# Kernel tuning notes

Hardware: AMD Instinct MI355X
Metric: run time of the kernel (lower is better)

## Reference

```python
import jax, jax.numpy as jnp
import numpy as np

B, L, D, H, A = 4, 2048, 1024, 16, 64  # batch, seq, d_model, n_head, d_head


def setup_inputs() -> dict:
    key = jax.random.key(0)
    ks = jax.random.split(key, 6)
    scale = 1.0 / np.sqrt(D)
    return {
        "xq": jax.random.normal(ks[0], (B, L, D), dtype=jnp.float32),
        "xkv": jax.random.normal(ks[1], (B, L, D), dtype=jnp.float32),
        "Q": jax.random.normal(ks[2], (D, H, A), dtype=jnp.float32) * scale,
        "K": jax.random.normal(ks[3], (D, H, A), dtype=jnp.float32) * scale,
        "V": jax.random.normal(ks[4], (D, H, A), dtype=jnp.float32) * scale,
        "O": jax.random.normal(ks[5], (D, H, A), dtype=jnp.float32) * scale,
    }


def reference(xq, xkv, Q, K, V, O):
    # embed: 'dha, ...ld -> ...lha'
    q = jnp.einsum('dha,bld->blha', Q, xq)
    k = jnp.einsum('dha,bld->blha', K, xkv)
    v = jnp.einsum('dha,bld->blha', V, xkv)
    # outer: '...lha, ...mha -> ...hlm'  (full LxL score matrix, no scaling in source)
    scores = jnp.einsum('blha,bmha->bhlm', q, k)
    attn = jax.nn.softmax(scores, axis=-1)  # dropout p=0 (eval)
    # score: '...hlm, ...mha -> ...lha'
    ctx = jnp.einsum('bhlm,bmha->blha', attn, v)
    # output: '...dha, ...lha -> ...ld'
    return jnp.einsum('dha,blha->bld', O, ctx)
```

## Files before the change

### kernel.cpp

```cpp
#include <hip/hip_runtime.h>
#include <math.h>

typedef __bf16 bf16;
typedef bf16 bf16x8 __attribute__((ext_vector_type(8)));
typedef bf16 bf16x4 __attribute__((ext_vector_type(4)));
typedef float f32x4 __attribute__((ext_vector_type(4)));
typedef float f32x16 __attribute__((ext_vector_type(16)));

#define B_ 4
#define L_ 2048
#define D_ 1024
#define H_ 16
#define A_ 64
#define HA_ 1024
#define BL_ 8192
#define LOG2E 1.44269504088896340736f

__device__ __forceinline__ void gload16(const void* g, void* l) {
  __builtin_amdgcn_global_load_lds((const __attribute__((address_space(1))) void*)g,
                                   (__attribute__((address_space(3))) void*)l,
                                   16, 0, 0);
}

__device__ __forceinline__ unsigned cvt_pk_bf16(float lo, float hi) {
  unsigned r;
  asm volatile("v_cvt_pk_bf16_f32 %0, %1, %2" : "=v"(r) : "v"(lo), "v"(hi));
  return r;
}

__device__ __forceinline__ void permswap(unsigned& a, unsigned& b) {
  asm volatile("v_permlane32_swap_b32 %0, %1" : "+v"(a), "+v"(b));
}

__device__ __forceinline__ void half_pair(float x, float& o1, float& o2) {
  unsigned a = __builtin_bit_cast(unsigned, x), b;
  asm volatile("v_mov_b32 %0, %1" : "=v"(b) : "v"(a));
  asm volatile("v_permlane32_swap_b32 %0, %1" : "+v"(a), "+v"(b));
  o1 = __builtin_bit_cast(float, a);
  o2 = __builtin_bit_cast(float, b);
}

__global__ __launch_bounds__(256) void cast_all(const float* __restrict__ xq,
                                                const float* __restrict__ xkv,
                                                const float* __restrict__ ow,
                                                bf16* __restrict__ xq_b,
                                                bf16* __restrict__ xkv_b,
                                                bf16* __restrict__ wo_b) {
  const int NX = BL_ * D_ / 8;
  const int NW = D_ * HA_ / 8;
  int i = blockIdx.x * blockDim.x + threadIdx.x;
  const float* src;
  bf16* dst;
  int j;
  if (i < NX) { src = xq; dst = xq_b; j = i; }
  else if (i < 2 * NX) { src = xkv; dst = xkv_b; j = i - NX; }
  else if (i < 2 * NX + NW) { src = ow; dst = wo_b; j = i - 2 * NX; }
  else return;
  const float4* s = reinterpret_cast<const float4*>(src) + (size_t)j * 2;
  float4 a = s[0], b = s[1];
  bf16x8 o;
  o[0] = (bf16)a.x; o[1] = (bf16)a.y; o[2] = (bf16)a.z; o[3] = (bf16)a.w;
  o[4] = (bf16)b.x; o[5] = (bf16)b.y; o[6] = (bf16)b.z; o[7] = (bf16)b.w;
  *reinterpret_cast<bf16x8*>(dst + (size_t)j * 8) = o;
}

__global__ __launch_bounds__(256) void transpose_cast_w3(const float* __restrict__ wq,
                                                         const float* __restrict__ wk,
                                                         const float* __restrict__ wv,
                                                         bf16* __restrict__ oq,
                                                         bf16* __restrict__ ok,
                                                         bf16* __restrict__ ov) {
  __shared__ float tile[32][33];
  const int z = blockIdx.z;
  const float* w = (z == 0) ? wq : (z == 1) ? wk : wv;
  bf16* wt = (z == 0) ? oq : (z == 1) ? ok : ov;
  const float scale = (z == 0) ? LOG2E : 1.0f;
  const int d0 = blockIdx.y * 32, h0 = blockIdx.x * 32;
  const int tx = threadIdx.x, ty = threadIdx.y;
  #pragma unroll
  for (int j = 0; j < 4; j++)
    tile[ty + j * 8][tx] = w[(size_t)(d0 + ty + j * 8) * HA_ + h0 + tx];
  __syncthreads();
  #pragma unroll
  for (int j = 0; j < 4; j++)
    wt[(size_t)(h0 + ty + j * 8) * D_ + d0 + tx] = (bf16)(tile[tx][ty + j * 8] * scale);
}

template <int MODE>
__device__ __forceinline__ void gemm_bt_core(const bf16* __restrict__ Ap,
                                             const bf16* __restrict__ Bp,
                                             void* __restrict__ Cp,
                                             int m0, int n0) {
  const int K = 1024;
  __shared__ __align__(16) bf16 As[128 * 32];
  __shared__ __align__(16) bf16 Bs[128 * 32];
  const int tid = threadIdx.x;
  const int lane = tid & 63, w = tid >> 6;
  const int wr = w >> 1, wc = w & 1;
  const int g = lane >> 4, c = lane & 15;
  f32x4 acc[4][4] = {};
  const int srow = tid >> 2, sch = tid & 3;
  const int sw0 = (sch ^ (srow & 3)) * 8;
  for (int k0 = 0; k0 < K; k0 += 32) {
    gload16(Ap + (size_t)(m0 + srow) * K + k0 + sw0, As + tid * 8);
    gload16(Ap + (size_t)(m0 + 64 + srow) * K + k0 + sw0, As + (256 + tid) * 8);
    gload16(Bp + (size_t)(n0 + srow) * K + k0 + sw0, Bs + tid * 8);
    gload16(Bp + (size_t)(n0 + 64 + srow) * K + k0 + sw0, Bs + (256 + tid) * 8);
    __syncthreads();
    bf16x8 af[4], bfr[4];
    #pragma unroll
    for (int m = 0; m < 4; m++)
      af[m] = *reinterpret_cast<const bf16x8*>(As + (wr * 64 + m * 16 + c) * 32 + ((g ^ (c & 3)) * 8));
    #pragma unroll
    for (int n = 0; n < 4; n++)
      bfr[n] = *reinterpret_cast<const bf16x8*>(Bs + (wc * 64 + n * 16 + c) * 32 + ((g ^ (c & 3)) * 8));
    #pragma unroll
    for (int m = 0; m < 4; m++)
      #pragma unroll
      for (int n = 0; n < 4; n++)
        acc[m][n] = __builtin_amdgcn_mfma_f32_16x16x32_bf16(af[m], bfr[n], acc[m][n], 0, 0, 0);
    __syncthreads();
  }
  #pragma unroll
  for (int m = 0; m < 4; m++) {
    #pragma unroll
    for (int n = 0; n < 4; n++) {
      if (MODE == 2) {
        int row0 = m0 + wr * 64 + m * 16 + g * 4;
        int col = n0 + wc * 64 + n * 16 + c;
        int b = row0 >> 11, l0 = row0 & 2047, h = col >> 6, a = col & 63;
        bf16x4 o4;
        #pragma unroll
        for (int i = 0; i < 4; i++) o4[i] = (bf16)acc[m][n][i];
        *reinterpret_cast<bf16x4*>((bf16*)Cp + ((size_t)(b * H_ + h) * A_ + a) * L_ + l0) = o4;
      } else {
        #pragma unroll
        for (int i = 0; i < 4; i++) {
          int row = m0 + wr * 64 + m * 16 + g * 4 + i;
          int col = n0 + wc * 64 + n * 16 + c;
          float v = acc[m][n][i];
          if (MODE == 0) {
            int b = row >> 11, l = row & 2047, h = col >> 6, a = col & 63;
            ((bf16*)Cp)[(((size_t)b * H_ + h) * L_ + l) * A_ + a] = (bf16)v;
          } else {
            ((float*)Cp)[(size_t)row * 1024 + col] = v;
          }
        }
      }
    }
  }
}

__device__ __forceinline__ void xcd_mn(int id, int& m0, int& n0) {
  int xcd = id & 7, j = id >> 3;
  m0 = (xcd * 8 + (j >> 3)) * 128;
  n0 = (j & 7) * 128;
}

__global__ __launch_bounds__(256, 2) void gemm_proj(const bf16* xq_b, const bf16* xkv_b,
                                                    const bf16* wq, const bf16* wk, const bf16* wv,
                                                    bf16* qb, bf16* kb, bf16* vtb) {
  int m0, n0;
  xcd_mn(blockIdx.x, m0, n0);
  const int z = blockIdx.z;
  if (z == 0)      gemm_bt_core<0>(xq_b, wq, qb, m0, n0);
  else if (z == 1) gemm_bt_core<0>(xkv_b, wk, kb, m0, n0);
  else             gemm_bt_core<2>(xkv_b, wv, vtb, m0, n0);
}

__global__ __launch_bounds__(256, 2) void gemm_out_k(const bf16* ctx, const bf16* wo, float* out) {
  int m0, n0;
  xcd_mn(blockIdx.x, m0, n0);
  gemm_bt_core<1>(ctx, wo, out, m0, n0);
}

__device__ __forceinline__ void pa_build(const f32x16& s, bf16x8& f0, bf16x8& f1) {
  #pragma unroll
  for (int sl = 0; sl < 2; sl++) {
    unsigned a0 = cvt_pk_bf16(s[8 * sl + 0], s[8 * sl + 1]);
    unsigned b0 = cvt_pk_bf16(s[8 * sl + 4], s[8 * sl + 5]);
    permswap(a0, b0);
    unsigned a1 = cvt_pk_bf16(s[8 * sl + 2], s[8 * sl + 3]);
    unsigned b1 = cvt_pk_bf16(s[8 * sl + 6], s[8 * sl + 7]);
    permswap(a1, b1);
    uint4 v; v.x = a0; v.y = a1; v.z = b0; v.w = b1;
    if (sl == 0) f0 = __builtin_bit_cast(bf16x8, v);
    else         f1 = __builtin_bit_cast(bf16x8, v);
  }
}

__global__ __launch_bounds__(512, 2) void attn_kernel(const bf16* __restrict__ qg,
                                                      const bf16* __restrict__ kg,
                                                      const bf16* __restrict__ vtg,
                                                      bf16* __restrict__ ctx) {
  __shared__ __align__(16) bf16 Ks[2][64 * 64];
  __shared__ __align__(16) bf16 Vs[2][64 * 64];
  const int tid = threadIdx.x;
  const int lane = tid & 63;
  const int w = tid >> 6;
  const int c = lane & 31;
  const int hi = lane >> 5;
  const int cs7 = c & 7;
  const int bh = blockIdx.x;
  const int q0 = blockIdx.y * 256;
  const bf16* qh = qg + (size_t)bh * L_ * A_;
  const bf16* kh = kg + (size_t)bh * L_ * A_;
  const bf16* vh = vtg + (size_t)bh * A_ * L_;

  const int qrow = q0 + w * 32 + c;
  bf16x8 qf[4];
  #pragma unroll
  for (int ds = 0; ds < 4; ds++)
    qf[ds] = *reinterpret_cast<const bf16x8*>(qh + (size_t)qrow * A_ + ds * 16 + hi * 8);

  f32x16 oacc0 = {}, oacc1 = {};
  float lrun = 0.f;

  int koA[4], koB[4];
  #pragma unroll
  for (int ds = 0; ds < 4; ds++) {
    koA[ds] = c * 64 + ((2 * ds + hi) ^ cs7) * 8;
    koB[ds] = (32 + c) * 64 + ((2 * ds + hi) ^ cs7) * 8;
  }

  const int sr = tid >> 3, sc = tid & 7;
  const int ss = (sc ^ (sr & 7)) * 8;
  const bf16* ksrc = kh + (size_t)sr * A_ + ss;
  const bf16* vsrc = vh + (size_t)sr * L_ + ss;

  gload16(ksrc, &Ks[0][tid * 8]);
  gload16(vsrc, &Vs[0][tid * 8]);
  __syncthreads();
  int cur = 0;

  for (int t = 0; t < L_ / 64; t++) {
    if (t < L_ / 64 - 1) {
      gload16(ksrc + (size_t)(t + 1) * 4096, &Ks[cur ^ 1][tid * 8]);
      gload16(vsrc + (size_t)(t + 1) * 64, &Vs[cur ^ 1][tid * 8]);
    }
    const bf16* Kc = Ks[cur];
    const bf16* Vc = Vs[cur];

    f32x16 s0 = {}, s1 = {};
    __builtin_amdgcn_s_setprio(1);
    #pragma unroll
    for (int ds = 0; ds < 4; ds++) {
      bf16x8 k0 = *reinterpret_cast<const bf16x8*>(Kc + koA[ds]);
      bf16x8 k1 = *reinterpret_cast<const bf16x8*>(Kc + koB[ds]);
      s0 = __builtin_amdgcn_mfma_f32_32x32x16_bf16(k0, qf[ds], s0, 0, 0, 0);
      s1 = __builtin_amdgcn_mfma_f32_32x32x16_bf16(k1, qf[ds], s1, 0, 0, 0);
    }
    __builtin_amdgcn_s_setprio(0);

    #pragma unroll
    for (int r = 0; r < 16; r++) {
      s0[r] = __builtin_amdgcn_exp2f(s0[r]);
      s1[r] = __builtin_amdgcn_exp2f(s1[r]);
    }

    float u0[8];
    #pragma unroll
    for (int r = 0; r < 8; r++)
      u0[r] = (s0[r] + s0[r + 8]) + (s1[r] + s1[r + 8]);
    float us = ((u0[0] + u0[1]) + (u0[2] + u0[3])) + ((u0[4] + u0[5]) + (u0[6] + u0[7]));
    float y1, y2;
    half_pair(us, y1, y2);
    lrun += y1 + y2;

    bf16x8 paf0, paf1, paf2, paf3;
    pa_build(s0, paf0, paf1);
    pa_build(s1, paf2, paf3);

    __builtin_amdgcn_s_setprio(1);
    #pragma unroll
    for (int ks = 0; ks < 4; ks++) {
      const bf16x8 pa = (ks == 0) ? paf0 : (ks == 1) ? paf1 : (ks == 2) ? paf2 : paf3;
      bf16x8 v0 = *reinterpret_cast<const bf16x8*>(Vc + koA[ks]);
      bf16x8 v1 = *reinterpret_cast<const bf16x8*>(Vc + koB[ks]);
      oacc0 = __builtin_amdgcn_mfma_f32_32x32x16_bf16(v0, pa, oacc0, 0, 0, 0);
      oacc1 = __builtin_amdgcn_mfma_f32_32x32x16_bf16(v1, pa, oacc1, 0, 0, 0);
    }
    __builtin_amdgcn_s_setprio(0);

    __syncthreads();
    cur ^= 1;
  }

  float inv = 1.f / lrun;
  const int b = bh >> 4, h = bh & 15;
  bf16* crow = ctx + (((size_t)b * L_ + qrow) * H_ + h) * A_;
  #pragma unroll
  for (int n = 0; n < 2; n++) {
    #pragma unroll
    for (int rq = 0; rq < 4; rq++) {
      bf16x4 o4;
      #pragma unroll
      for (int j = 0; j < 4; j++) {
        float v = (n == 0) ? oacc0[rq * 4 + j] : oacc1[rq * 4 + j];
        o4[j] = (bf16)(v * inv);
      }
      *reinterpret_cast<bf16x4*>(crow + n * 32 + rq * 8 + hi * 4) = o4;
    }
  }
}

extern "C" void kernel_launch(void* const* d_in, const int* in_sizes, int n_in,
                              void* d_out, int out_size, void* d_ws, size_t ws_size,
                              hipStream_t stream) {
  const float* xq = (const float*)d_in[0];
  const float* xkv = (const float*)d_in[1];
  const float* Qw = (const float*)d_in[2];
  const float* Kw = (const float*)d_in[3];
  const float* Vw = (const float*)d_in[4];
  const float* Ow = (const float*)d_in[5];
  float* out = (float*)d_out;

  char* ws = (char*)d_ws;
  const size_t SZ16 = (size_t)BL_ * HA_ * sizeof(bf16);
  const size_t SZW = (size_t)D_ * HA_ * sizeof(bf16);
  bf16* xq_b = (bf16*)(ws);
  bf16* xkv_b = (bf16*)(ws + SZ16);
  bf16* wq_t = (bf16*)(ws + 2 * SZ16);
  bf16* wk_t = (bf16*)(ws + 2 * SZ16 + SZW);
  bf16* wv_t = (bf16*)(ws + 2 * SZ16 + 2 * SZW);
  bf16* wo_b = (bf16*)(ws + 2 * SZ16 + 3 * SZW);
  bf16* qb = (bf16*)(ws + 2 * SZ16 + 4 * SZW);
  bf16* kb = qb + (size_t)BL_ * HA_;
  bf16* vtb = kb + (size_t)BL_ * HA_;
  bf16* ctxb = xkv_b;

  const int NCAST = (2 * BL_ * D_ + D_ * HA_) / 8;
  cast_all<<<(NCAST + 255) / 256, 256, 0, stream>>>(xq, xkv, Ow, xq_b, xkv_b, wo_b);
  transpose_cast_w3<<<dim3(32, 32, 3), dim3(32, 8), 0, stream>>>(Qw, Kw, Vw, wq_t, wk_t, wv_t);

  gemm_proj<<<dim3(512, 1, 3), 256, 0, stream>>>(xq_b, xkv_b, wq_t, wk_t, wv_t, qb, kb, vtb);
  attn_kernel<<<dim3(64, 8), 512, 0, stream>>>(qb, kb, vtb, ctxb);
  gemm_out_k<<<512, 256, 0, stream>>>(ctxb, wo_b, out);
}
```

Measured before the change: 192.3 us.

## Process two 32-row query tiles per wave in attention, halving block threads

The attention kernel now uses 256 threads per block, and each wave handles 64 query rows as two 32-row halves instead of 32 rows. Each K/V fragment read from LDS is reused for twice as many MFMAs, and each thread stages two 16-byte chunks of K and of V per tile. This cuts LDS read traffic and the number of waves per block synchronizing per tile. In exchange, register pressure per thread roughly doubles (accumulators and score tiles), which may hurt occupancy or cause spills.

```diff
diff --git a/kernel.cpp b/kernel.cpp
--- a/kernel.cpp
+++ b/kernel.cpp
@@ -189,7 +189,7 @@
   }
 }
 
-__global__ __launch_bounds__(512, 2) void attn_kernel(const bf16* __restrict__ qg,
+__global__ __launch_bounds__(256, 2) void attn_kernel(const bf16* __restrict__ qg,
                                                       const bf16* __restrict__ kg,
                                                       const bf16* __restrict__ vtg,
                                                       bf16* __restrict__ ctx) {
@@ -207,14 +207,18 @@
   const bf16* kh = kg + (size_t)bh * L_ * A_;
   const bf16* vh = vtg + (size_t)bh * A_ * L_;
 
-  const int qrow = q0 + w * 32 + c;
-  bf16x8 qf[4];
-  #pragma unroll
-  for (int ds = 0; ds < 4; ds++)
-    qf[ds] = *reinterpret_cast<const bf16x8*>(qh + (size_t)qrow * A_ + ds * 16 + hi * 8);
-
-  f32x16 oacc0 = {}, oacc1 = {};
-  float lrun = 0.f;
+  const int qrowL = q0 + w * 64 + c;
+  const int qrowH = qrowL + 32;
+  bf16x8 qfL[4], qfH[4];
+  #pragma unroll
+  for (int ds = 0; ds < 4; ds++) {
+    qfL[ds] = *reinterpret_cast<const bf16x8*>(qh + (size_t)qrowL * A_ + ds * 16 + hi * 8);
+    qfH[ds] = *reinterpret_cast<const bf16x8*>(qh + (size_t)qrowH * A_ + ds * 16 + hi * 8);
+  }
+
+  f32x16 oA0 = {}, oA1 = {};
+  f32x16 oB0 = {}, oB1 = {};
+  float lrunL = 0.f, lrunH = 0.f;
 
   int koA[4], koB[4];
   #pragma unroll
@@ -225,60 +229,81 @@
 
   const int sr = tid >> 3, sc = tid & 7;
   const int ss = (sc ^ (sr & 7)) * 8;
-  const bf16* ksrc = kh + (size_t)sr * A_ + ss;
-  const bf16* vsrc = vh + (size_t)sr * L_ + ss;
-
-  gload16(ksrc, &Ks[0][tid * 8]);
-  gload16(vsrc, &Vs[0][tid * 8]);
+  const bf16* ksrc0 = kh + (size_t)sr * A_ + ss;
+  const bf16* ksrc1 = kh + (size_t)(sr + 32) * A_ + ss;
+  const bf16* vsrc0 = vh + (size_t)sr * L_ + ss;
+  const bf16* vsrc1 = vh + (size_t)(sr + 32) * L_ + ss;
+
+  auto stage = [&](int buf, int t) {
+    gload16(ksrc0 + (size_t)t * 4096, &Ks[buf][tid * 8]);
+    gload16(ksrc1 + (size_t)t * 4096, &Ks[buf][2048 + tid * 8]);
+    gload16(vsrc0 + (size_t)t * 64, &Vs[buf][tid * 8]);
+    gload16(vsrc1 + (size_t)t * 64, &Vs[buf][2048 + tid * 8]);
+  };
+
+  stage(0, 0);
   __syncthreads();
   int cur = 0;
 
   for (int t = 0; t < L_ / 64; t++) {
-    if (t < L_ / 64 - 1) {
-      gload16(ksrc + (size_t)(t + 1) * 4096, &Ks[cur ^ 1][tid * 8]);
-      gload16(vsrc + (size_t)(t + 1) * 64, &Vs[cur ^ 1][tid * 8]);
-    }
+    if (t < L_ / 64 - 1) stage(cur ^ 1, t + 1);
     const bf16* Kc = Ks[cur];
     const bf16* Vc = Vs[cur];
 
-    f32x16 s0 = {}, s1 = {};
+    f32x16 sA0 = {}, sA1 = {}, sB0 = {}, sB1 = {};
     __builtin_amdgcn_s_setprio(1);
     #pragma unroll
     for (int ds = 0; ds < 4; ds++) {
       bf16x8 k0 = *reinterpret_cast<const bf16x8*>(Kc + koA[ds]);
       bf16x8 k1 = *reinterpret_cast<const bf16x8*>(Kc + koB[ds]);
-      s0 = __builtin_amdgcn_mfma_f32_32x32x16_bf16(k0, qf[ds], s0, 0, 0, 0);
-      s1 = __builtin_amdgcn_mfma_f32_32x32x16_bf16(k1, qf[ds], s1, 0, 0, 0);
+      sA0 = __builtin_amdgcn_mfma_f32_32x32x16_bf16(k0, qfL[ds], sA0, 0, 0, 0);
+      sA1 = __builtin_amdgcn_mfma_f32_32x32x16_bf16(k1, qfL[ds], sA1, 0, 0, 0);
+      sB0 = __builtin_amdgcn_mfma_f32_32x32x16_bf16(k0, qfH[ds], sB0, 0, 0, 0);
+      sB1 = __builtin_amdgcn_mfma_f32_32x32x16_bf16(k1, qfH[ds], sB1, 0, 0, 0);
     }
     __builtin_amdgcn_s_setprio(0);
 
     #pragma unroll
     for (int r = 0; r < 16; r++) {
-      s0[r] = __builtin_amdgcn_exp2f(s0[r]);
-      s1[r] = __builtin_amdgcn_exp2f(s1[r]);
-    }
-
-    float u0[8];
-    #pragma unroll
-    for (int r = 0; r < 8; r++)
-      u0[r] = (s0[r] + s0[r + 8]) + (s1[r] + s1[r + 8]);
-    float us = ((u0[0] + u0[1]) + (u0[2] + u0[3])) + ((u0[4] + u0[5]) + (u0[6] + u0[7]));
-    float y1, y2;
-    half_pair(us, y1, y2);
-    lrun += y1 + y2;
-
-    bf16x8 paf0, paf1, paf2, paf3;
-    pa_build(s0, paf0, paf1);
-    pa_build(s1, paf2, paf3);
+      sA0[r] = __builtin_amdgcn_exp2f(sA0[r]);
+      sA1[r] = __builtin_amdgcn_exp2f(sA1[r]);
+      sB0[r] = __builtin_amdgcn_exp2f(sB0[r]);
+      sB1[r] = __builtin_amdgcn_exp2f(sB1[r]);
+    }
+
+    {
+      float u0[8], v0[8];
+      #pragma unroll
+      for (int r = 0; r < 8; r++) {
+        u0[r] = (sA0[r] + sA0[r + 8]) + (sA1[r] + sA1[r + 8]);
+        v0[r] = (sB0[r] + sB0[r + 8]) + (sB1[r] + sB1[r + 8]);
+      }
+      float us = ((u0[0] + u0[1]) + (u0[2] + u0[3])) + ((u0[4] + u0[5]) + (u0[6] + u0[7]));
+      float vs = ((v0[0] + v0[1]) + (v0[2] + v0[3])) + ((v0[4] + v0[5]) + (v0[6] + v0[7]));
+      float y1, y2, z1, z2;
+      half_pair(us, y1, y2);
+      half_pair(vs, z1, z2);
+      lrunL += y1 + y2;
+      lrunH += z1 + z2;
+    }
+
+    bf16x8 paA0, paA1, paA2, paA3, paB0, paB1, paB2, paB3;
+    pa_build(sA0, paA0, paA1);
+    pa_build(sA1, paA2, paA3);
+    pa_build(sB0, paB0, paB1);
+    pa_build(sB1, paB2, paB3);
 
     __builtin_amdgcn_s_setprio(1);
     #pragma unroll
     for (int ks = 0; ks < 4; ks++) {
-      const bf16x8 pa = (ks == 0) ? paf0 : (ks == 1) ? paf1 : (ks == 2) ? paf2 : paf3;
+      const bf16x8 pa = (ks == 0) ? paA0 : (ks == 1) ? paA1 : (ks == 2) ? paA2 : paA3;
+      const bf16x8 pb = (ks == 0) ? paB0 : (ks == 1) ? paB1 : (ks == 2) ? paB2 : paB3;
       bf16x8 v0 = *reinterpret_cast<const bf16x8*>(Vc + koA[ks]);
       bf16x8 v1 = *reinterpret_cast<const bf16x8*>(Vc + koB[ks]);
-      oacc0 = __builtin_amdgcn_mfma_f32_32x32x16_bf16(v0, pa, oacc0, 0, 0, 0);
-      oacc1 = __builtin_amdgcn_mfma_f32_32x32x16_bf16(v1, pa, oacc1, 0, 0, 0);
+      oA0 = __builtin_amdgcn_mfma_f32_32x32x16_bf16(v0, pa, oA0, 0, 0, 0);
+      oA1 = __builtin_amdgcn_mfma_f32_32x32x16_bf16(v1, pa, oA1, 0, 0, 0);
+      oB0 = __builtin_amdgcn_mfma_f32_32x32x16_bf16(v0, pb, oB0, 0, 0, 0);
+      oB1 = __builtin_amdgcn_mfma_f32_32x32x16_bf16(v1, pb, oB1, 0, 0, 0);
     }
     __builtin_amdgcn_s_setprio(0);
 
@@ -286,21 +311,38 @@
     cur ^= 1;
   }
 
-  float inv = 1.f / lrun;
   const int b = bh >> 4, h = bh & 15;
-  bf16* crow = ctx + (((size_t)b * L_ + qrow) * H_ + h) * A_;
-  #pragma unroll
-  for (int n = 0; n < 2; n++) {
-    #pragma unroll
-    for (int rq = 0; rq < 4; rq++) {
-      bf16x4 o4;
+  {
+    float inv = 1.f / lrunL;
+    bf16* crow = ctx + (((size_t)b * L_ + qrowL) * H_ + h) * A_;
+    #pragma unroll
+    for (int n = 0; n < 2; n++)
       #pragma unroll
-      for (int j = 0; j < 4; j++) {
-        float v = (n == 0) ? oacc0[rq * 4 + j] : oacc1[rq * 4 + j];
-        o4[j] = (bf16)(v * inv);
+      for (int rq = 0; rq < 4; rq++) {
+        bf16x4 o4;
+        #pragma unroll
+        for (int j = 0; j < 4; j++) {
+          float v = (n == 0) ? oA0[rq * 4 + j] : oA1[rq * 4 + j];
+          o4[j] = (bf16)(v * inv);
+        }
+        *reinterpret_cast<bf16x4*>(crow + n * 32 + rq * 8 + hi * 4) = o4;
       }
-      *reinterpret_cast<bf16x4*>(crow + n * 32 + rq * 8 + hi * 4) = o4;
-    }
+  }
+  {
+    float inv = 1.f / lrunH;
+    bf16* crow = ctx + (((size_t)b * L_ + qrowH) * H_ + h) * A_;
+    #pragma unroll
+    for (int n = 0; n < 2; n++)
+      #pragma unroll
+      for (int rq = 0; rq < 4; rq++) {
+        bf16x4 o4;
+        #pragma unroll
+        for (int j = 0; j < 4; j++) {
+          float v = (n == 0) ? oB0[rq * 4 + j] : oB1[rq * 4 + j];
+          o4[j] = (bf16)(v * inv);
+        }
+        *reinterpret_cast<bf16x4*>(crow + n * 32 + rq * 8 + hi * 4) = o4;
+      }
   }
 }
 
@@ -334,6 +376,6 @@
   transpose_cast_w3<<<dim3(32, 32, 3), dim3(32, 8), 0, stream>>>(Qw, Kw, Vw, wq_t, wk_t, wv_t);
 
   gemm_proj<<<dim3(512, 1, 3), 256, 0, stream>>>(xq_b, xkv_b, wq_t, wk_t, wv_t, qb, kb, vtb);
-  attn_kernel<<<dim3(64, 8), 512, 0, stream>>>(qb, kb, vtb, ctxb);
+  attn_kernel<<<dim3(64, 8), 256, 0, stream>>>(qb, kb, vtb, ctxb);
   gemm_out_k<<<512, 256, 0, stream>>>(ctxb, wo_b, out);
 }
```

After: 193.5 us. Within noise of the previous version (+0.6%).

## Compute softmax row sums via MFMA with ones and double-step K/V pipeline

Applied to the files above, without the earlier changes.

Replaces the VALU reduction and permlane swap for the softmax denominator with an extra MFMA that multiplies the bf16 probability tile by a ones matrix, accumulating row sums in a 16-wide register tile. The K/V LDS ring grows from two to four buffers and the loop now handles two 64-key tiles per barrier, halving the number of __syncthreads. In exchange it adds one MFMA per k-step (about 50% more PV-stage MFMAs), sixteen more accumulator registers, and doubles the LDS footprint. The denominator now sums bf16-rounded probabilities instead of fp32 values.

```diff
diff --git a/kernel.cpp b/kernel.cpp
--- a/kernel.cpp
+++ b/kernel.cpp
@@ -30,14 +30,6 @@
 
 __device__ __forceinline__ void permswap(unsigned& a, unsigned& b) {
   asm volatile("v_permlane32_swap_b32 %0, %1" : "+v"(a), "+v"(b));
-}
-
-__device__ __forceinline__ void half_pair(float x, float& o1, float& o2) {
-  unsigned a = __builtin_bit_cast(unsigned, x), b;
-  asm volatile("v_mov_b32 %0, %1" : "=v"(b) : "v"(a));
-  asm volatile("v_permlane32_swap_b32 %0, %1" : "+v"(a), "+v"(b));
-  o1 = __builtin_bit_cast(float, a);
-  o2 = __builtin_bit_cast(float, b);
 }
 
 __global__ __launch_bounds__(256) void cast_all(const float* __restrict__ xq,
@@ -193,8 +185,8 @@
                                                       const bf16* __restrict__ kg,
                                                       const bf16* __restrict__ vtg,
                                                       bf16* __restrict__ ctx) {
-  __shared__ __align__(16) bf16 Ks[2][64 * 64];
-  __shared__ __align__(16) bf16 Vs[2][64 * 64];
+  __shared__ __align__(16) bf16 Ks[4][64 * 64];
+  __shared__ __align__(16) bf16 Vs[4][64 * 64];
   const int tid = threadIdx.x;
   const int lane = tid & 63;
   const int w = tid >> 6;
@@ -213,8 +205,12 @@
   for (int ds = 0; ds < 4; ds++)
     qf[ds] = *reinterpret_cast<const bf16x8*>(qh + (size_t)qrow * A_ + ds * 16 + hi * 8);
 
+  bf16x8 ones;
+  #pragma unroll
+  for (int j = 0; j < 8; j++) ones[j] = (bf16)1.0f;
+
   f32x16 oacc0 = {}, oacc1 = {};
-  float lrun = 0.f;
+  f32x16 ssum = {};
 
   int koA[4], koB[4];
   #pragma unroll
@@ -228,19 +224,15 @@
   const bf16* ksrc = kh + (size_t)sr * A_ + ss;
   const bf16* vsrc = vh + (size_t)sr * L_ + ss;
 
-  gload16(ksrc, &Ks[0][tid * 8]);
-  gload16(vsrc, &Vs[0][tid * 8]);
-  __syncthreads();
-  int cur = 0;
-
-  for (int t = 0; t < L_ / 64; t++) {
-    if (t < L_ / 64 - 1) {
-      gload16(ksrc + (size_t)(t + 1) * 4096, &Ks[cur ^ 1][tid * 8]);
-      gload16(vsrc + (size_t)(t + 1) * 64, &Vs[cur ^ 1][tid * 8]);
-    }
-    const bf16* Kc = Ks[cur];
-    const bf16* Vc = Vs[cur];
-
+  auto stage = [&](int t) {
+    int buf = t & 3;
+    gload16(ksrc + (size_t)t * 4096, &Ks[buf][tid * 8]);
+    gload16(vsrc + (size_t)t * 64, &Vs[buf][tid * 8]);
+  };
+
+  auto compute = [&](int t) {
+    const bf16* Kc = Ks[t & 3];
+    const bf16* Vc = Vs[t & 3];
     f32x16 s0 = {}, s1 = {};
     __builtin_amdgcn_s_setprio(1);
     #pragma unroll
@@ -257,15 +249,6 @@
       s0[r] = __builtin_amdgcn_exp2f(s0[r]);
       s1[r] = __builtin_amdgcn_exp2f(s1[r]);
     }
-
-    float u0[8];
-    #pragma unroll
-    for (int r = 0; r < 8; r++)
-      u0[r] = (s0[r] + s0[r + 8]) + (s1[r] + s1[r + 8]);
-    float us = ((u0[0] + u0[1]) + (u0[2] + u0[3])) + ((u0[4] + u0[5]) + (u0[6] + u0[7]));
-    float y1, y2;
-    half_pair(us, y1, y2);
-    lrun += y1 + y2;
 
     bf16x8 paf0, paf1, paf2, paf3;
     pa_build(s0, paf0, paf1);
@@ -279,14 +262,27 @@
       bf16x8 v1 = *reinterpret_cast<const bf16x8*>(Vc + koB[ks]);
       oacc0 = __builtin_amdgcn_mfma_f32_32x32x16_bf16(v0, pa, oacc0, 0, 0, 0);
       oacc1 = __builtin_amdgcn_mfma_f32_32x32x16_bf16(v1, pa, oacc1, 0, 0, 0);
+      ssum = __builtin_amdgcn_mfma_f32_32x32x16_bf16(ones, pa, ssum, 0, 0, 0);
     }
     __builtin_amdgcn_s_setprio(0);
-
+  };
+
+  stage(0);
+  stage(1);
+  __syncthreads();
+
+  for (int p = 0; p < L_ / 128; p++) {
+    int t0 = 2 * p;
+    if (t0 + 2 < L_ / 64) {
+      stage(t0 + 2);
+      stage(t0 + 3);
+    }
+    compute(t0);
+    compute(t0 + 1);
     __syncthreads();
-    cur ^= 1;
-  }
-
-  float inv = 1.f / lrun;
+  }
+
+  float inv = 1.f / ssum[0];
   const int b = bh >> 4, h = bh & 15;
   bf16* crow = ctx + (((size_t)b * L_ + qrow) * H_ + h) * A_;
   #pragma unroll
```

After: 197.8 us. 2.9% more time.
